# Kernel optimization log

Hardware: AMD Instinct MI355X
Metric: run time of the kernel (lower is better)

## Reference

```python
import jax, jax.numpy as jnp
import numpy as np

B, S, D, H = 2, 2048, 2048, 16
HD = D // H

def setup_inputs() -> dict:
    key = jax.random.key(0)
    ks = jax.random.split(key, 6)
    x = jax.random.normal(ks[0], (B, S, D), dtype=jnp.float32)
    # causal mask: 1 where attention allowed, 0 where masked
    mask = jnp.tril(jnp.ones((S, S), dtype=jnp.int32))[None, None, :, :]
    scale_w = 0.02
    W_qkv = jax.random.normal(ks[1], (D, 3 * D), dtype=jnp.float32) * scale_w
    b_qkv = jnp.zeros((3 * D,), dtype=jnp.float32)
    W_proj = jax.random.normal(ks[2], (D, D), dtype=jnp.float32) * scale_w
    b_proj = jnp.zeros((D,), dtype=jnp.float32)
    return {"x": x, "W_qkv": W_qkv, "b_qkv": b_qkv, "W_proj": W_proj, "b_proj": b_proj, "mask": mask}

def reference(x, W_qkv, b_qkv, W_proj, b_proj, mask):
    b, s, d = x.shape
    qkv = x @ W_qkv + b_qkv                       # [b,s,3d]
    qkv = qkv.reshape(b, s, 3, H, HD)
    q = jnp.transpose(qkv[:, :, 0], (0, 2, 1, 3))  # [b,h,s,hd]
    k = jnp.transpose(qkv[:, :, 1], (0, 2, 1, 3))
    v = jnp.transpose(qkv[:, :, 2], (0, 2, 1, 3))
    scale = HD ** -0.5
    attn = jnp.einsum('bhqd,bhkd->bhqk', q, k) * scale
    attn = jnp.where(mask == 0, -jnp.inf, attn)
    attn = jax.nn.softmax(attn, axis=-1)
    # dropout is identity in eval mode
    out = jnp.einsum('bhqk,bhkd->bhqd', attn, v)   # [b,h,s,hd]
    out = jnp.transpose(out, (0, 2, 1, 3)).reshape(b, s, d)
    return out @ W_proj + b_proj
```

## Files before the change

kernel.cpp:

```cpp
#include <hip/hip_runtime.h>
#include <hip/hip_bf16.h>
#include <math.h>

#define BATCH 2
#define SEQ   2048
#define DIM   2048
#define NH    16
#define HD    128
#define QKV_N (3 * DIM)
#define TOKENS (BATCH * SEQ)

typedef __attribute__((ext_vector_type(8))) short bf16x8;
typedef __attribute__((ext_vector_type(4))) float f32x4;

typedef __attribute__((address_space(1))) const void* as1cv;
typedef __attribute__((address_space(3))) void* as3v;

__device__ __forceinline__ short f2bf(float x) {
    unsigned u = __float_as_uint(x);
    u += 0x7fffu + ((u >> 16) & 1u);
    return (short)(u >> 16);
}

__device__ __forceinline__ float bf2f(short x) {
    return __uint_as_float(((unsigned)(unsigned short)x) << 16);
}

__device__ __forceinline__ void gload16(const short* g, short* lds) {
    __builtin_amdgcn_global_load_lds((as1cv)g, (as3v)lds, 16, 0, 0);
}

__global__ __launch_bounds__(256)
void f32_to_bf16_kernel(const float* __restrict__ in, short* __restrict__ out) {
    const size_t i = ((size_t)blockIdx.x * 256 + threadIdx.x) * 8;
    const float4 a = *reinterpret_cast<const float4*>(in + i);
    const float4 b = *reinterpret_cast<const float4*>(in + i + 4);
    bf16x8 v;
    v[0] = f2bf(a.x); v[1] = f2bf(a.y); v[2] = f2bf(a.z); v[3] = f2bf(a.w);
    v[4] = f2bf(b.x); v[5] = f2bf(b.y); v[6] = f2bf(b.z); v[7] = f2bf(b.w);
    *reinterpret_cast<bf16x8*>(out + i) = v;
}

__global__ __launch_bounds__(256)
void transpose_f32_to_bf16(const float* __restrict__ W, short* __restrict__ Wt,
                           int K, int N) {
    __shared__ float t[64][65];
    const int tid = threadIdx.x;
    const int n0 = blockIdx.x * 64;
    const int k0 = blockIdx.y * 64;
    const int tc = tid & 63, tr = tid >> 6;
    #pragma unroll
    for (int i = 0; i < 16; ++i)
        t[tr + i * 4][tc] = W[(size_t)(k0 + tr + i * 4) * N + n0 + tc];
    __syncthreads();
    #pragma unroll
    for (int i = 0; i < 16; ++i)
        Wt[(size_t)(n0 + tr + i * 4) * K + k0 + tc] = f2bf(t[tc][tr + i * 4]);
}

template <bool BF16OUT>
__global__ __launch_bounds__(256, 2)
void gemm_mfma_kernel(const short* __restrict__ A, const short* __restrict__ Bt,
                      const float* __restrict__ bias, void* __restrict__ Cv,
                      int M, int N, int K, int nM) {
    __shared__ short A_lds[2][128 * 64];
    __shared__ short B_lds[2][128 * 64];

    const int tid  = threadIdx.x;
    const int lane = tid & 63;
    const int w    = tid >> 6;
    const int lr   = lane & 15;
    const int lhi  = lane >> 4;
    const int wr   = w >> 1;
    const int wc   = w & 1;

    const int nwg  = gridDim.x;
    const int cpx  = nwg >> 3;
    const int orig = blockIdx.x;
    const int wg   = (orig & 7) * cpx + (orig >> 3);
    const int bm   = (wg % nM) * 128;
    const int bn   = (wg / nM) * 128;

    const int srow   = tid >> 3;
    const int schunk = (tid & 7) ^ (srow & 7);
    const short* gA = A  + (size_t)(bm + srow) * K + schunk * 8;
    const short* gB = Bt + (size_t)(bn + srow) * K + schunk * 8;

    const int nt = K >> 6;

    auto STAGE = [&](int t, int buf) {
        const int ko = t * 64;
        short* la = &A_lds[buf][w * 512];
        short* lb = &B_lds[buf][w * 512];
        #pragma unroll
        for (int i = 0; i < 4; ++i)
            gload16(gA + (size_t)(i * 32) * K + ko, la + i * 2048);
        #pragma unroll
        for (int i = 0; i < 4; ++i)
            gload16(gB + (size_t)(i * 32) * K + ko, lb + i * 2048);
    };

    f32x4 acc[4][4] = {};

    STAGE(0, 0);
    STAGE(1, 1);
    asm volatile("s_waitcnt vmcnt(8)" ::: "memory");
    __builtin_amdgcn_s_barrier();

    int cur = 0;
    for (int t = 0; t < nt; ++t, cur ^= 1) {
        bf16x8 af[2][4], bfr[2][4];
        const short* Ab = &A_lds[cur][0];
        const short* Bb = &B_lds[cur][0];
        #pragma unroll
        for (int ks = 0; ks < 2; ++ks) {
            const int cb = ks * 4 + lhi;
            #pragma unroll
            for (int mi = 0; mi < 4; ++mi) {
                const int r = wr * 64 + mi * 16 + lr;
                af[ks][mi] = *reinterpret_cast<const bf16x8*>(
                    &Ab[r * 64 + ((cb ^ (r & 7)) << 3)]);
            }
            #pragma unroll
            for (int ni = 0; ni < 4; ++ni) {
                const int c = wc * 64 + ni * 16 + lr;
                bfr[ks][ni] = *reinterpret_cast<const bf16x8*>(
                    &Bb[c * 64 + ((cb ^ (c & 7)) << 3)]);
            }
        }
        asm volatile("s_waitcnt lgkmcnt(0)" ::: "memory");
        __builtin_amdgcn_sched_barrier(0);
        __builtin_amdgcn_s_barrier();
        __builtin_amdgcn_sched_barrier(0);

        if (t + 2 < nt) STAGE(t + 2, cur);

        __builtin_amdgcn_s_setprio(1);
        #pragma unroll
        for (int ks = 0; ks < 2; ++ks)
            #pragma unroll
            for (int mi = 0; mi < 4; ++mi)
                #pragma unroll
                for (int ni = 0; ni < 4; ++ni)
                    acc[mi][ni] = __builtin_amdgcn_mfma_f32_16x16x32_bf16(
                        af[ks][mi], bfr[ks][ni], acc[mi][ni], 0, 0, 0);
        __builtin_amdgcn_s_setprio(0);
        __builtin_amdgcn_sched_barrier(0);

        if (t + 2 < nt) {
            asm volatile("s_waitcnt vmcnt(8)" ::: "memory");
            __builtin_amdgcn_s_barrier();
        } else if (t + 1 < nt) {
            asm volatile("s_waitcnt vmcnt(0)" ::: "memory");
            __builtin_amdgcn_s_barrier();
        }
    }

    #pragma unroll
    for (int mi = 0; mi < 4; ++mi) {
        #pragma unroll
        for (int j = 0; j < 4; ++j) {
            const int r = bm + wr * 64 + mi * 16 + lhi * 4 + j;
            #pragma unroll
            for (int ni = 0; ni < 4; ++ni) {
                const int c = bn + wc * 64 + ni * 16 + lr;
                const float v = acc[mi][ni][j] + bias[c];
                if (BF16OUT) ((short*)Cv)[(size_t)r * N + c] = f2bf(v);
                else         ((float*)Cv)[(size_t)r * N + c] = v;
            }
        }
    }
}

__device__ __forceinline__ int swz8(int row) {
    return ((row ^ (row >> 2)) & 7) << 3;
}

__global__ __launch_bounds__(256)
void attn_mfma_kernel(const short* __restrict__ qkv, short* __restrict__ out) {
    __shared__ short K_lds[64 * 128];
    __shared__ short V_lds[128 * 64];
    __shared__ short P_lds[4 * 16 * 64];

    const int tid  = threadIdx.x;
    const int lane = tid & 63;
    const int w    = tid >> 6;

    const int z    = blockIdx.x;
    const int qblk = (SEQ / 64 - 1) - (z >> 5);
    const int bh   = z & 31;
    const int h    = bh & 15;
    const int b    = bh >> 4;

    const int q0 = qblk * 64;
    const size_t tokbase = (size_t)b * SEQ * QKV_N;

    const int lr  = lane & 15;
    const int lhi = lane >> 4;
    const float lg2scale = 0.1275174468658922f;

    const int qrow = q0 + w * 16 + lr;
    const short* qrowp = qkv + tokbase + (size_t)qrow * QKV_N + h * HD;
    bf16x8 qfrag[4];
    #pragma unroll
    for (int ks = 0; ks < 4; ++ks) {
        bf16x8 v = *reinterpret_cast<const bf16x8*>(qrowp + ks * 32 + lhi * 8);
        bf16x8 sv;
        #pragma unroll
        for (int e = 0; e < 8; ++e) sv[e] = f2bf(bf2f(v[e]) * lg2scale);
        qfrag[ks] = sv;
    }

    bf16x8 ones8;
    #pragma unroll
    for (int e = 0; e < 8; ++e) ones8[e] = (short)0x3F80;

    f32x4 o[8] = {};
    f32x4 lacc = {};

    const int wq0 = q0 + w * 16;
    const int ntiles = qblk + 1;

    const int krow16 = tid >> 4;
    const int kch    = tid & 15;

    for (int t = 0; t < ntiles; ++t) {
        {
            const short* kb = qkv + tokbase + (size_t)(t * 64) * QKV_N + DIM + h * HD;
            #pragma unroll
            for (int i = 0; i < 4; ++i) {
                const int row = i * 16 + krow16;
                const int sch = (kch & 8) | ((kch & 7) ^ ((row ^ (row >> 2)) & 7));
                gload16(kb + (size_t)row * QKV_N + sch * 8,
                        &K_lds[(i * 16 + w * 4) * 128]);
            }
        }
        {
            const int p  = tid >> 3;
            const int c  = tid & 7;
            const int kv = p * 2;
            const int kc = kv >> 3;
            const short* vrow = qkv + tokbase + (size_t)(t * 64 + kv) * QKV_N
                                + 2 * DIM + h * HD + c * 16;
            #pragma unroll
            for (int half = 0; half < 2; ++half) {
                const bf16x8 va = *reinterpret_cast<const bf16x8*>(vrow + half * 8);
                const bf16x8 vb = *reinterpret_cast<const bf16x8*>(vrow + QKV_N + half * 8);
                #pragma unroll
                for (int dd = 0; dd < 8; ++dd) {
                    const int d  = c * 16 + half * 8 + dd;
                    const int sw = ((d >> 4) ^ d) & 7;
                    const unsigned pk = ((unsigned)(unsigned short)va[dd]) |
                                        (((unsigned)(unsigned short)vb[dd]) << 16);
                    *reinterpret_cast<unsigned*>(
                        &V_lds[d * 64 + ((kc ^ sw) << 3) + (kv & 7)]) = pk;
                }
            }
        }
        __syncthreads();

        f32x4 s[4] = {};
        #pragma unroll
        for (int ks = 0; ks < 4; ++ks) {
            #pragma unroll
            for (int cg = 0; cg < 4; ++cg) {
                const int row = cg * 16 + lr;
                const bf16x8 kf = *reinterpret_cast<const bf16x8*>(
                    &K_lds[row * 128 + ((ks * 32 + lhi * 8) ^ swz8(row))]);
                s[cg] = __builtin_amdgcn_mfma_f32_16x16x32_bf16(qfrag[ks], kf, s[cg], 0, 0, 0);
            }
        }

        const bool dmask = (t == qblk);
        short* pbase = &P_lds[w * 1024];
        #pragma unroll
        for (int cg = 0; cg < 4; ++cg) {
            const int kvg = t * 64 + cg * 16 + lr;
            const int cx  = cg * 16 + lr;
            #pragma unroll
            for (int j = 0; j < 4; ++j) {
                float sv = s[cg][j];
                if (dmask && (kvg > wq0 + lhi * 4 + j)) sv = -1.0e38f;
                sv = exp2f(fminf(sv, 80.f));
                const int rw = lhi * 4 + j;
                pbase[rw * 64 + (cx ^ swz8(rw))] = f2bf(sv);
            }
        }
        bf16x8 pa[2];
        #pragma unroll
        for (int ks = 0; ks < 2; ++ks)
            pa[ks] = *reinterpret_cast<const bf16x8*>(
                &pbase[lr * 64 + ((ks * 32 + lhi * 8) ^ swz8(lr))]);

        #pragma unroll
        for (int cg = 0; cg < 8; ++cg) {
            const int d  = cg * 16 + lr;
            const int sw = ((d >> 4) ^ d) & 7;
            #pragma unroll
            for (int ks = 0; ks < 2; ++ks) {
                const bf16x8 vf = *reinterpret_cast<const bf16x8*>(
                    &V_lds[d * 64 + (((ks * 4 + lhi) ^ sw) << 3)]);
                o[cg] = __builtin_amdgcn_mfma_f32_16x16x32_bf16(pa[ks], vf, o[cg], 0, 0, 0);
            }
        }
        #pragma unroll
        for (int ks = 0; ks < 2; ++ks)
            lacc = __builtin_amdgcn_mfma_f32_16x16x32_bf16(pa[ks], ones8, lacc, 0, 0, 0);

        __syncthreads();
    }

    #pragma unroll
    for (int j = 0; j < 4; ++j) {
        const float inv = 1.f / lacc[j];
        const int qg = q0 + w * 16 + lhi * 4 + j;
        short* op = out + (size_t)(b * SEQ + qg) * DIM + h * HD;
        #pragma unroll
        for (int cg = 0; cg < 8; ++cg)
            op[cg * 16 + lr] = f2bf(o[cg][j] * inv);
    }
}

extern "C" void kernel_launch(void* const* d_in, const int* in_sizes, int n_in,
                              void* d_out, int out_size, void* d_ws, size_t ws_size,
                              hipStream_t stream) {
    const float* x      = (const float*)d_in[0];
    const float* W_qkv  = (const float*)d_in[1];
    const float* b_qkv  = (const float*)d_in[2];
    const float* W_proj = (const float*)d_in[3];
    const float* b_proj = (const float*)d_in[4];

    float* out = (float*)d_out;

    short* qkv_bf  = (short*)d_ws;
    short* attn_bf = qkv_bf  + (size_t)TOKENS * QKV_N;
    short* x_bf    = attn_bf + (size_t)TOKENS * DIM;
    short* wqkv_t  = x_bf    + (size_t)TOKENS * DIM;
    short* wproj_t = wqkv_t  + (size_t)DIM * QKV_N;

    f32_to_bf16_kernel<<<TOKENS * DIM / (256 * 8), 256, 0, stream>>>(x, x_bf);
    {
        dim3 g(QKV_N / 64, DIM / 64);
        transpose_f32_to_bf16<<<g, 256, 0, stream>>>(W_qkv, wqkv_t, DIM, QKV_N);
    }
    {
        dim3 g(DIM / 64, DIM / 64);
        transpose_f32_to_bf16<<<g, 256, 0, stream>>>(W_proj, wproj_t, DIM, DIM);
    }

    {
        const int nM = TOKENS / 128, nN = QKV_N / 128;
        gemm_mfma_kernel<true><<<nM * nN, 256, 0, stream>>>(
            x_bf, wqkv_t, b_qkv, (void*)qkv_bf, TOKENS, QKV_N, DIM, nM);
    }
    attn_mfma_kernel<<<BATCH * NH * (SEQ / 64), 256, 0, stream>>>(qkv_bf, attn_bf);

    {
        const int nM = TOKENS / 128, nN = DIM / 128;
        gemm_mfma_kernel<false><<<nM * nN, 256, 0, stream>>>(
            attn_bf, wproj_t, b_proj, (void*)out, TOKENS, DIM, DIM, nM);
    }
}
```

Before: 247.6 us.

## Use 256x128 tiles with 512 threads and triple-buffered LDS in GEMMs

```diff
diff --git a/kernel.cpp b/kernel.cpp
--- a/kernel.cpp
+++ b/kernel.cpp
@@ -58,27 +58,28 @@
         Wt[(size_t)(n0 + tr + i * 4) * K + k0 + tc] = f2bf(t[tc][tr + i * 4]);
 }
 
+#define BUFSH 24576
+
 template <bool BF16OUT>
-__global__ __launch_bounds__(256, 2)
-void gemm_mfma_kernel(const short* __restrict__ A, const short* __restrict__ Bt,
-                      const float* __restrict__ bias, void* __restrict__ Cv,
-                      int M, int N, int K, int nM) {
-    __shared__ short A_lds[2][128 * 64];
-    __shared__ short B_lds[2][128 * 64];
+__global__ __launch_bounds__(512, 2)
+void gemm_mfma3_kernel(const short* __restrict__ A, const short* __restrict__ Bt,
+                       const float* __restrict__ bias, void* __restrict__ Cv,
+                       int M, int N, int K, int nM) {
+    __shared__ short lds[3 * BUFSH];
 
     const int tid  = threadIdx.x;
     const int lane = tid & 63;
-    const int w    = tid >> 6;
+    const int wv   = tid >> 6;
     const int lr   = lane & 15;
     const int lhi  = lane >> 4;
-    const int wr   = w >> 1;
-    const int wc   = w & 1;
+    const int wr   = wv & 3;
+    const int wc   = wv >> 2;
 
     const int nwg  = gridDim.x;
     const int cpx  = nwg >> 3;
     const int orig = blockIdx.x;
     const int wg   = (orig & 7) * cpx + (orig >> 3);
-    const int bm   = (wg % nM) * 128;
+    const int bm   = (wg % nM) * 256;
     const int bn   = (wg / nM) * 128;
 
     const int srow   = tid >> 3;
@@ -90,28 +91,29 @@
 
     auto STAGE = [&](int t, int buf) {
         const int ko = t * 64;
-        short* la = &A_lds[buf][w * 512];
-        short* lb = &B_lds[buf][w * 512];
+        short* la = &lds[buf * BUFSH + wv * 512];
+        short* lb = &lds[buf * BUFSH + 16384 + wv * 512];
         #pragma unroll
         for (int i = 0; i < 4; ++i)
-            gload16(gA + (size_t)(i * 32) * K + ko, la + i * 2048);
-        #pragma unroll
-        for (int i = 0; i < 4; ++i)
-            gload16(gB + (size_t)(i * 32) * K + ko, lb + i * 2048);
+            gload16(gA + (size_t)(i * 64) * K + ko, la + i * 4096);
+        #pragma unroll
+        for (int i = 0; i < 2; ++i)
+            gload16(gB + (size_t)(i * 64) * K + ko, lb + i * 4096);
     };
 
     f32x4 acc[4][4] = {};
 
-    STAGE(0, 0);
-    STAGE(1, 1);
-    asm volatile("s_waitcnt vmcnt(8)" ::: "memory");
+    STAGE(0, 0); STAGE(1, 1); STAGE(2, 2);
+    __builtin_amdgcn_sched_barrier(0);
+    asm volatile("s_waitcnt vmcnt(12)" ::: "memory");
     __builtin_amdgcn_s_barrier();
-
-    int cur = 0;
-    for (int t = 0; t < nt; ++t, cur ^= 1) {
+    __builtin_amdgcn_sched_barrier(0);
+
+    int buf = 0;
+    for (int t = 0; t < nt; ++t) {
+        const short* Ab = &lds[buf * BUFSH];
+        const short* Bb = &lds[buf * BUFSH + 16384];
         bf16x8 af[2][4], bfr[2][4];
-        const short* Ab = &A_lds[cur][0];
-        const short* Bb = &B_lds[cur][0];
         #pragma unroll
         for (int ks = 0; ks < 2; ++ks) {
             const int cb = ks * 4 + lhi;
@@ -128,13 +130,6 @@
                     &Bb[c * 64 + ((cb ^ (c & 7)) << 3)]);
             }
         }
-        asm volatile("s_waitcnt lgkmcnt(0)" ::: "memory");
-        __builtin_amdgcn_sched_barrier(0);
-        __builtin_amdgcn_s_barrier();
-        __builtin_amdgcn_sched_barrier(0);
-
-        if (t + 2 < nt) STAGE(t + 2, cur);
-
         __builtin_amdgcn_s_setprio(1);
         #pragma unroll
         for (int ks = 0; ks < 2; ++ks)
@@ -145,15 +140,26 @@
                     acc[mi][ni] = __builtin_amdgcn_mfma_f32_16x16x32_bf16(
                         af[ks][mi], bfr[ks][ni], acc[mi][ni], 0, 0, 0);
         __builtin_amdgcn_s_setprio(0);
+
+        asm volatile("s_waitcnt lgkmcnt(0)" ::: "memory");
         __builtin_amdgcn_sched_barrier(0);
-
-        if (t + 2 < nt) {
-            asm volatile("s_waitcnt vmcnt(8)" ::: "memory");
+        __builtin_amdgcn_s_barrier();
+        __builtin_amdgcn_sched_barrier(0);
+
+        if (t + 3 < nt) {
+            STAGE(t + 3, buf);
+            __builtin_amdgcn_sched_barrier(0);
+            asm volatile("s_waitcnt vmcnt(12)" ::: "memory");
+            __builtin_amdgcn_s_barrier();
+        } else if (t + 2 < nt) {
+            asm volatile("s_waitcnt vmcnt(6)" ::: "memory");
             __builtin_amdgcn_s_barrier();
         } else if (t + 1 < nt) {
             asm volatile("s_waitcnt vmcnt(0)" ::: "memory");
             __builtin_amdgcn_s_barrier();
         }
+        __builtin_amdgcn_sched_barrier(0);
+        buf = (buf == 2) ? 0 : buf + 1;
     }
 
     #pragma unroll
@@ -349,15 +355,15 @@
     }
 
     {
-        const int nM = TOKENS / 128, nN = QKV_N / 128;
-        gemm_mfma_kernel<true><<<nM * nN, 256, 0, stream>>>(
+        const int nM = TOKENS / 256, nN = QKV_N / 128;
+        gemm_mfma3_kernel<true><<<nM * nN, 512, 0, stream>>>(
             x_bf, wqkv_t, b_qkv, (void*)qkv_bf, TOKENS, QKV_N, DIM, nM);
     }
     attn_mfma_kernel<<<BATCH * NH * (SEQ / 64), 256, 0, stream>>>(qkv_bf, attn_bf);
 
     {
-        const int nM = TOKENS / 128, nN = DIM / 128;
-        gemm_mfma_kernel<false><<<nM * nN, 256, 0, stream>>>(
+        const int nM = TOKENS / 256, nN = DIM / 128;
+        gemm_mfma3_kernel<false><<<nM * nN, 512, 0, stream>>>(
             attn_bf, wproj_t, b_proj, (void*)out, TOKENS, DIM, DIM, nM);
     }
 }
```

Measured after the change: 264.5 us. +6.8%, slower.
